# Kernel optimization log

Measured on AMD Instinct MI355X. Metric: run time of the kernel, lower is better.

Reference implementation:

```python
import jax, jax.numpy as jnp
import numpy as np

NEG_SLOPE = 0.2  # PyG GATConv default negative_slope

def gat_layer(x, src, dst, W, a_src, a_dst, bias, n_nodes):
    # x: [N, F_in]; W: [F_in, H*C]; a_src/a_dst: [H, C]; bias: [H*C]
    H, C = a_src.shape
    h = (x @ W).reshape(n_nodes, H, C)                      # [N, H, C]
    al_src = jnp.sum(h * a_src, axis=-1)                    # [N, H]
    al_dst = jnp.sum(h * a_dst, axis=-1)                    # [N, H]
    e = jax.nn.leaky_relu(al_src[src] + al_dst[dst], NEG_SLOPE)  # [E, H]
    # segment softmax over destination nodes (every node has a self loop)
    m = jax.ops.segment_max(e, dst, num_segments=n_nodes)  # [N, H]
    ex = jnp.exp(e - m[dst])
    denom = jax.ops.segment_sum(ex, dst, num_segments=n_nodes)  # [N, H]
    alpha = ex / denom[dst]                                 # [E, H]
    out = jax.ops.segment_sum(h[src] * alpha[:, :, None], dst, num_segments=n_nodes)  # [N, H, C]
    return out.reshape(n_nodes, H * C) + bias


def setup_inputs() -> dict:
    key = jax.random.key(0)
    ks = jax.random.split(key, 10)
    N, E, F_in, H, Ch, Co = 50000, 800000, 128, 4, 32, 8
    s = lambda fan: 1.0 / np.sqrt(fan)
    return {
        "x": jax.random.normal(ks[0], (N, F_in), dtype=jnp.float32),
        "edge_index": jax.random.randint(ks[1], (2, E), 0, N, dtype=jnp.int64),
        "W1": jax.random.normal(ks[2], (F_in, H * Ch), dtype=jnp.float32) * s(F_in),
        "att_src1": jax.random.normal(ks[3], (H, Ch), dtype=jnp.float32) * s(Ch),
        "att_dst1": jax.random.normal(ks[4], (H, Ch), dtype=jnp.float32) * s(Ch),
        "bias1": jnp.zeros((H * Ch,), dtype=jnp.float32),
        "W2": jax.random.normal(ks[5], (H * Ch, H * Co), dtype=jnp.float32) * s(H * Ch),
        "att_src2": jax.random.normal(ks[6], (H, Co), dtype=jnp.float32) * s(Co),
        "att_dst2": jax.random.normal(ks[7], (H, Co), dtype=jnp.float32) * s(Co),
        "bias2": jnp.zeros((H * Co,), dtype=jnp.float32),
    }


def reference(x, edge_index, W1, att_src1, att_dst1, bias1, W2, att_src2, att_dst2, bias2):
    n = x.shape[0]
    loop = jnp.arange(n, dtype=edge_index.dtype)  # add_self_loops=True (PyG default)
    src = jnp.concatenate([edge_index[0], loop])
    dst = jnp.concatenate([edge_index[1], loop])
    h = jax.nn.relu(gat_layer(x, src, dst, W1, att_src1, att_dst1, bias1, n))
    # F.dropout(p=0.6, training=False) -> identity in eval mode
    out = gat_layer(h, src, dst, W2, att_src2, att_dst2, bias2, n)
    return jax.nn.log_softmax(out, axis=1)
```

## Files before the change

### kernel.cpp

```cpp
#include <hip/hip_runtime.h>
#include <hip/hip_fp16.h>

struct alignas(8) Half4 { __half2 lo; __half2 hi; };

#define MAXDEG 64


__global__ void k_fill(const int* __restrict__ ei, int E, int N,
                       int* __restrict__ cursor, unsigned short* __restrict__ adj) {
  int e = blockIdx.x * blockDim.x + threadIdx.x;
  int Et = E + N;
  if (e >= Et) return;
  int s, d;
  if (e < E) { s = ei[e]; d = ei[E + e]; } else { s = d = e - E; }
  int pos = atomicAdd(&cursor[d], 1);
  if (pos < MAXDEG) adj[(size_t)d * MAXDEG + pos] = (unsigned short)s;
}


#define XS_STRIDE 33

__global__ void __launch_bounds__(256) k_gemm1(
    const float* __restrict__ x, const float* __restrict__ W,
    const float* __restrict__ as, const float* __restrict__ ad,
    __half* __restrict__ h1h, float* __restrict__ als,
    float* __restrict__ ald, int N) {
  __shared__ float4 xs[64 * XS_STRIDE];
  int t = threadIdx.x;
  int base = blockIdx.x * 64;
  const float4* x4 = (const float4*)x;
  #pragma unroll
  for (int i = 0; i < 8; ++i) {
    int idx = t + i * 256;
    int n = idx >> 5, k4 = idx & 31;
    int gn = base + n; if (gn >= N) gn = N - 1;
    xs[n * XS_STRIDE + k4] = x4[gn * 32 + k4];
  }
  __syncthreads();

  int c4 = t & 31, nr = t >> 5;
  const float4* w4 = (const float4*)W;
  float4 acc[8];
  #pragma unroll
  for (int i = 0; i < 8; ++i) acc[i] = make_float4(0.f, 0.f, 0.f, 0.f);

  for (int k4 = 0; k4 < 32; ++k4) {
    float4 w0 = w4[(k4 * 4 + 0) * 32 + c4];
    float4 w1 = w4[(k4 * 4 + 1) * 32 + c4];
    float4 w2 = w4[(k4 * 4 + 2) * 32 + c4];
    float4 w3 = w4[(k4 * 4 + 3) * 32 + c4];
    #pragma unroll
    for (int i = 0; i < 8; ++i) {
      float4 xv = xs[(nr * 8 + i) * XS_STRIDE + k4];
      acc[i].x += xv.x * w0.x + xv.y * w1.x + xv.z * w2.x + xv.w * w3.x;
      acc[i].y += xv.x * w0.y + xv.y * w1.y + xv.z * w2.y + xv.w * w3.y;
      acc[i].z += xv.x * w0.z + xv.y * w1.z + xv.z * w2.z + xv.w * w3.z;
      acc[i].w += xv.x * w0.w + xv.y * w1.w + xv.z * w2.w + xv.w * w3.w;
    }
  }

  int hh = c4 >> 3;
  int cl = (c4 & 7) * 4;
  float a10 = as[hh * 32 + cl], a11 = as[hh * 32 + cl + 1],
        a12 = as[hh * 32 + cl + 2], a13 = as[hh * 32 + cl + 3];
  float a20 = ad[hh * 32 + cl], a21 = ad[hh * 32 + cl + 1],
        a22 = ad[hh * 32 + cl + 2], a23 = ad[hh * 32 + cl + 3];
  Half4* h1p = (Half4*)h1h;
  #pragma unroll
  for (int i = 0; i < 8; ++i) {
    int gn = base + nr * 8 + i;
    float ps = acc[i].x * a10 + acc[i].y * a11 + acc[i].z * a12 + acc[i].w * a13;
    float pd = acc[i].x * a20 + acc[i].y * a21 + acc[i].z * a22 + acc[i].w * a23;
    ps += __shfl_xor(ps, 1); pd += __shfl_xor(pd, 1);
    ps += __shfl_xor(ps, 2); pd += __shfl_xor(pd, 2);
    ps += __shfl_xor(ps, 4); pd += __shfl_xor(pd, 4);
    if (gn < N) {
      Half4 hv;
      hv.lo = __floats2half2_rn(acc[i].x, acc[i].y);
      hv.hi = __floats2half2_rn(acc[i].z, acc[i].w);
      h1p[gn * 32 + c4] = hv;
      if ((c4 & 7) == 0) { als[gn * 4 + hh] = ps; ald[gn * 4 + hh] = pd; }
    }
  }
}


__global__ void __launch_bounds__(256) k_gemm2(
    const __half* __restrict__ hin, const float* __restrict__ W,
    const float* __restrict__ as, const float* __restrict__ ad,
    __half* __restrict__ h2h, float* __restrict__ als,
    float* __restrict__ ald, int N) {
  __shared__ float4 xs[64 * XS_STRIDE];
  __shared__ float2 ws[128 * 16];
  int t = threadIdx.x;
  int base = blockIdx.x * 64;
  const uint2* xg = (const uint2*)hin;
  #pragma unroll
  for (int i = 0; i < 8; ++i) {
    int idx = t + i * 256;
    int n = idx >> 5, k4 = idx & 31;
    int gn = base + n; if (gn >= N) gn = N - 1;
    uint2 u = xg[gn * 32 + k4];
    __half2 a = *(const __half2*)&u.x;
    __half2 b = *(const __half2*)&u.y;
    float2 fa = __half22float2(a), fb = __half22float2(b);
    xs[n * XS_STRIDE + k4] = make_float4(fa.x, fa.y, fb.x, fb.y);
  }
  const float2* w2g = (const float2*)W;
  #pragma unroll
  for (int i = 0; i < 8; ++i) ws[t + i * 256] = w2g[t + i * 256];
  __syncthreads();

  int c2 = t & 15, nr = t >> 4;
  float2 acc[4];
  #pragma unroll
  for (int i = 0; i < 4; ++i) acc[i] = make_float2(0.f, 0.f);

  #pragma unroll 4
  for (int k4 = 0; k4 < 32; ++k4) {
    float2 w0 = ws[(k4 * 4 + 0) * 16 + c2];
    float2 w1 = ws[(k4 * 4 + 1) * 16 + c2];
    float2 w2v = ws[(k4 * 4 + 2) * 16 + c2];
    float2 w3 = ws[(k4 * 4 + 3) * 16 + c2];
    #pragma unroll
    for (int i = 0; i < 4; ++i) {
      float4 xv = xs[(nr * 4 + i) * XS_STRIDE + k4];
      acc[i].x += xv.x * w0.x + xv.y * w1.x + xv.z * w2v.x + xv.w * w3.x;
      acc[i].y += xv.x * w0.y + xv.y * w1.y + xv.z * w2v.y + xv.w * w3.y;
    }
  }

  int hh = c2 >> 2;
  int cl = (c2 & 3) * 2;
  float a10 = as[hh * 8 + cl], a11 = as[hh * 8 + cl + 1];
  float a20 = ad[hh * 8 + cl], a21 = ad[hh * 8 + cl + 1];
  __half2* h2p = (__half2*)h2h;
  #pragma unroll
  for (int i = 0; i < 4; ++i) {
    int gn = base + nr * 4 + i;
    float ps = acc[i].x * a10 + acc[i].y * a11;
    float pd = acc[i].x * a20 + acc[i].y * a21;
    ps += __shfl_xor(ps, 1); pd += __shfl_xor(pd, 1);
    ps += __shfl_xor(ps, 2); pd += __shfl_xor(pd, 2);
    if (gn < N) {
      h2p[gn * 16 + c2] = __floats2half2_rn(acc[i].x, acc[i].y);
      if ((c2 & 3) == 0) { als[gn * 4 + hh] = ps; ald[gn * 4 + hh] = pd; }
    }
  }
}


__global__ void k_agg1(const int* __restrict__ degp, const unsigned short* __restrict__ adj,
                       const __half* __restrict__ h1h, const float* __restrict__ als,
                       const float* __restrict__ ald, const float* __restrict__ bias,
                       __half* __restrict__ outh, int N) {
  int wid = (blockIdx.x * blockDim.x + threadIdx.x) >> 6;
  int lane = threadIdx.x & 63;
  if (wid >= N) return;
  int h = lane >> 4;
  int hb = h * 4;
  int jw = lane & 3, hw = (lane >> 2) & 3;
  float aldw = ald[wid * 4 + hw];
  float aldo = ald[wid * 4 + h];
  int deg = degp[wid]; if (deg > MAXDEG) deg = MAXDEG;
  const unsigned short* arow = adj + (size_t)wid * MAXDEG;
  float acc0 = 0.f, acc1 = 0.f, wsum = 0.f;
  const __half2* h1v = (const __half2*)h1h;
  int p = 0;
  for (; p + 3 < deg; p += 4) {
    int sj = arow[p + jw];
    int s0 = __shfl(sj, 0), s1 = __shfl(sj, 1), s2 = __shfl(sj, 2), s3 = __shfl(sj, 3);
    float2 v0 = __half22float2(h1v[s0 * 64 + lane]);
    float2 v1 = __half22float2(h1v[s1 * 64 + lane]);
    float2 v2 = __half22float2(h1v[s2 * 64 + lane]);
    float2 v3 = __half22float2(h1v[s3 * 64 + lane]);
    float ew = als[sj * 4 + hw] + aldw;
    ew = (ew > 0.f) ? ew : 0.2f * ew;
    float w = __expf(ew);
    float w0 = __shfl(w, hb + 0), w1 = __shfl(w, hb + 1),
          w2 = __shfl(w, hb + 2), w3 = __shfl(w, hb + 3);
    wsum += (w0 + w1) + (w2 + w3);
    acc0 += w0 * v0.x + w1 * v1.x + w2 * v2.x + w3 * v3.x;
    acc1 += w0 * v0.y + w1 * v1.y + w2 * v2.y + w3 * v3.y;
  }
  for (; p < deg; ++p) {
    int s0 = arow[p];
    float e0 = als[s0 * 4 + h] + aldo;
    e0 = (e0 > 0.f) ? e0 : 0.2f * e0;
    float w0 = __expf(e0);
    float2 v0 = __half22float2(h1v[s0 * 64 + lane]);
    wsum += w0;
    acc0 += w0 * v0.x;
    acc1 += w0 * v0.y;
  }
  float inv = 1.f / wsum;
  float o0 = fmaxf(acc0 * inv + bias[lane * 2 + 0], 0.f);
  float o1 = fmaxf(acc1 * inv + bias[lane * 2 + 1], 0.f);
  ((__half2*)outh)[wid * 64 + lane] = __floats2half2_rn(o0, o1);
}


__global__ void k_agg2(const int* __restrict__ degp, const unsigned short* __restrict__ adj,
                       const __half* __restrict__ h2h, const float* __restrict__ als,
                       const float* __restrict__ ald, const float* __restrict__ bias,
                       float* __restrict__ out, int N) {
  int tid = blockIdx.x * blockDim.x + threadIdx.x;
  int node = tid >> 5;
  int sl = threadIdx.x & 31;
  if (node >= N) return;
  int h = sl >> 3;
  int hb = h * 4;
  int jw = sl & 3, hw = (sl >> 2) & 3;
  float aldw = ald[node * 4 + hw];
  float aldo = ald[node * 4 + h];
  int deg = degp[node]; if (deg > MAXDEG) deg = MAXDEG;
  const unsigned short* arow = adj + (size_t)node * MAXDEG;
  float acc = 0.f, wsum = 0.f;
  int p = 0;
  for (; p + 3 < deg; p += 4) {
    int sj = arow[p + jw];
    int s0 = __shfl(sj, 0, 32), s1 = __shfl(sj, 1, 32),
        s2 = __shfl(sj, 2, 32), s3 = __shfl(sj, 3, 32);
    float x0 = __half2float(h2h[s0 * 32 + sl]);
    float x1 = __half2float(h2h[s1 * 32 + sl]);
    float x2 = __half2float(h2h[s2 * 32 + sl]);
    float x3 = __half2float(h2h[s3 * 32 + sl]);
    float ew = als[sj * 4 + hw] + aldw;
    ew = (ew > 0.f) ? ew : 0.2f * ew;
    float w = __expf(ew);
    float w0 = __shfl(w, hb + 0, 32), w1 = __shfl(w, hb + 1, 32),
          w2 = __shfl(w, hb + 2, 32), w3 = __shfl(w, hb + 3, 32);
    wsum += (w0 + w1) + (w2 + w3);
    acc += (w0 * x0 + w1 * x1) + (w2 * x2 + w3 * x3);
  }
  for (; p < deg; ++p) {
    int s0 = arow[p];
    float e0 = als[s0 * 4 + h] + aldo;
    e0 = (e0 > 0.f) ? e0 : 0.2f * e0;
    float w0 = __expf(e0);
    wsum += w0;
    acc += w0 * __half2float(h2h[s0 * 32 + sl]);
  }
  float val = acc / wsum + bias[sl];
  float m = val;
  for (int off = 16; off; off >>= 1) m = fmaxf(m, __shfl_xor(m, off, 32));
  float ex = __expf(val - m);
  float ssum = ex;
  for (int off = 16; off; off >>= 1) ssum += __shfl_xor(ssum, off, 32);
  out[node * 32 + sl] = val - m - __logf(ssum);
}


extern "C" void kernel_launch(void* const* d_in, const int* in_sizes, int n_in,
                              void* d_out, int out_size, void* d_ws, size_t ws_size,
                              hipStream_t stream) {
  const float* x   = (const float*)d_in[0];
  const int*   ei  = (const int*)d_in[1];
  const float* W1  = (const float*)d_in[2];
  const float* as1 = (const float*)d_in[3];
  const float* ad1 = (const float*)d_in[4];
  const float* b1  = (const float*)d_in[5];
  const float* W2  = (const float*)d_in[6];
  const float* as2 = (const float*)d_in[7];
  const float* ad2 = (const float*)d_in[8];
  const float* b2  = (const float*)d_in[9];
  float* outp = (float*)d_out;

  int N  = in_sizes[0] / 128;
  int E  = in_sizes[1] / 2;
  int Et = E + N;

  char* wsp = (char*)d_ws;
  size_t off = 0;
  auto alloc = [&](size_t bytes) -> void* {
    void* p = wsp + off;
    off += (bytes + 255) & ~(size_t)255;
    return p;
  };
  int*            cursor = (int*)alloc((size_t)N * 4);
  unsigned short* adj    = (unsigned short*)alloc((size_t)N * MAXDEG * 2);
  __half*         h1     = (__half*)alloc((size_t)N * 128 * 2);
  float*          al1s   = (float*)alloc((size_t)N * 4 * 4);
  float*          al1d   = (float*)alloc((size_t)N * 4 * 4);
  __half*         h2in   = (__half*)alloc((size_t)N * 128 * 2);
  __half*         h2     = (__half*)alloc((size_t)N * 32 * 2);
  float*          al2s   = (float*)alloc((size_t)N * 4 * 4);
  float*          al2d   = (float*)alloc((size_t)N * 4 * 4);

  hipMemsetAsync(cursor, 0, (size_t)N * 4, stream);

  int eb = (Et + 255) / 256;
  k_fill<<<eb, 256, 0, stream>>>(ei, E, N, cursor, adj);

  int gb = (N + 63) / 64;
  k_gemm1<<<gb, 256, 0, stream>>>(x, W1, as1, ad1, h1, al1s, al1d, N);
  k_agg1 <<<(N + 3) / 4, 256, 0, stream>>>(cursor, adj, h1, al1s, al1d, b1, h2in, N);
  k_gemm2<<<gb, 256, 0, stream>>>(h2in, W2, as2, ad2, h2, al2s, al2d, N);
  k_agg2 <<<(N + 7) / 8, 256, 0, stream>>>(cursor, adj, h2, al2s, al2d, b2, outp, N);
}
```

Measured before the change: 177.5 us.

## Fuse adjacency fill into gemm1 and layer-1 aggregation into gemm2

Adjacency construction runs as extra blocks of the first GEMM launch, removing a separate launch. Layer-1 aggregation is computed per block into shared memory and fed directly into the layer-2 GEMM, removing the h2in intermediate round trip through global memory and one launch. In exchange, each wave now aggregates 16 nodes serially, which reduces the number of independent gather waves in flight.

```diff
diff --git a/kernel.cpp b/kernel.cpp
--- a/kernel.cpp
+++ b/kernel.cpp
@@ -4,30 +4,32 @@
 struct alignas(8) Half4 { __half2 lo; __half2 hi; };
 
 #define MAXDEG 64
-
-
-__global__ void k_fill(const int* __restrict__ ei, int E, int N,
-                       int* __restrict__ cursor, unsigned short* __restrict__ adj) {
-  int e = blockIdx.x * blockDim.x + threadIdx.x;
-  int Et = E + N;
-  if (e >= Et) return;
-  int s, d;
-  if (e < E) { s = ei[e]; d = ei[E + e]; } else { s = d = e - E; }
-  int pos = atomicAdd(&cursor[d], 1);
-  if (pos < MAXDEG) adj[(size_t)d * MAXDEG + pos] = (unsigned short)s;
-}
-
-
 #define XS_STRIDE 33
 
-__global__ void __launch_bounds__(256) k_gemm1(
+
+__global__ void __launch_bounds__(256) k_fg1(
+    const int* __restrict__ ei, int E, int N, int gb,
+    int* __restrict__ cursor, unsigned short* __restrict__ adj,
     const float* __restrict__ x, const float* __restrict__ W,
     const float* __restrict__ as, const float* __restrict__ ad,
-    __half* __restrict__ h1h, float* __restrict__ als,
-    float* __restrict__ ald, int N) {
+    __half* __restrict__ h1h, float* __restrict__ als, float* __restrict__ ald) {
   __shared__ float4 xs[64 * XS_STRIDE];
+  int b = blockIdx.x;
   int t = threadIdx.x;
-  int base = blockIdx.x * 64;
+
+  if (b >= gb) {
+    int e = (b - gb) * 256 + t;
+    int Et = E + N;
+    if (e < Et) {
+      int s, d;
+      if (e < E) { s = ei[e]; d = ei[E + e]; } else { s = d = e - E; }
+      int pos = atomicAdd(&cursor[d], 1);
+      if (pos < MAXDEG) adj[(size_t)d * MAXDEG + pos] = (unsigned short)s;
+    }
+    return;
+  }
+
+  int base = b * 64;
   const float4* x4 = (const float4*)x;
   #pragma unroll
   for (int i = 0; i < 8; ++i) {
@@ -85,30 +87,71 @@
 }
 
 
-__global__ void __launch_bounds__(256) k_gemm2(
-    const __half* __restrict__ hin, const float* __restrict__ W,
-    const float* __restrict__ as, const float* __restrict__ ad,
-    __half* __restrict__ h2h, float* __restrict__ als,
-    float* __restrict__ ald, int N) {
+__global__ void __launch_bounds__(256) k_ag12(
+    const int* __restrict__ degp, const unsigned short* __restrict__ adj,
+    const __half* __restrict__ h1h, const float* __restrict__ als1,
+    const float* __restrict__ ald1, const float* __restrict__ b1,
+    const float* __restrict__ W2,
+    const float* __restrict__ as2, const float* __restrict__ ad2,
+    __half* __restrict__ h2h, float* __restrict__ als2,
+    float* __restrict__ ald2, int N) {
   __shared__ float4 xs[64 * XS_STRIDE];
   __shared__ float2 ws[128 * 16];
   int t = threadIdx.x;
   int base = blockIdx.x * 64;
-  const uint2* xg = (const uint2*)hin;
-  #pragma unroll
-  for (int i = 0; i < 8; ++i) {
-    int idx = t + i * 256;
-    int n = idx >> 5, k4 = idx & 31;
-    int gn = base + n; if (gn >= N) gn = N - 1;
-    uint2 u = xg[gn * 32 + k4];
-    __half2 a = *(const __half2*)&u.x;
-    __half2 b = *(const __half2*)&u.y;
-    float2 fa = __half22float2(a), fb = __half22float2(b);
-    xs[n * XS_STRIDE + k4] = make_float4(fa.x, fa.y, fb.x, fb.y);
-  }
-  const float2* w2g = (const float2*)W;
+
+  const float2* w2g = (const float2*)W2;
   #pragma unroll
   for (int i = 0; i < 8; ++i) ws[t + i * 256] = w2g[t + i * 256];
+
+  int lane = t & 63, wv = t >> 6;
+  int h = lane >> 4;
+  int hb = h * 4;
+  int jw = lane & 3, hw = (lane >> 2) & 3;
+  const __half2* h1v = (const __half2*)h1h;
+  float2* xs2 = (float2*)xs;
+  float bs0 = b1[lane * 2 + 0], bs1 = b1[lane * 2 + 1];
+
+  for (int i = 0; i < 16; ++i) {
+    int ln = wv * 16 + i;
+    int node = base + ln; if (node >= N) node = N - 1;
+    float aldw = ald1[node * 4 + hw];
+    float aldo = ald1[node * 4 + h];
+    int deg = degp[node]; if (deg > MAXDEG) deg = MAXDEG;
+    const unsigned short* arow = adj + (size_t)node * MAXDEG;
+    float acc0 = 0.f, acc1 = 0.f, wsum = 0.f;
+    int p = 0;
+    for (; p + 3 < deg; p += 4) {
+      int sj = arow[p + jw];
+      int s0 = __shfl(sj, 0), s1 = __shfl(sj, 1), s2 = __shfl(sj, 2), s3 = __shfl(sj, 3);
+      float2 v0 = __half22float2(h1v[s0 * 64 + lane]);
+      float2 v1 = __half22float2(h1v[s1 * 64 + lane]);
+      float2 v2 = __half22float2(h1v[s2 * 64 + lane]);
+      float2 v3 = __half22float2(h1v[s3 * 64 + lane]);
+      float ew = als1[sj * 4 + hw] + aldw;
+      ew = (ew > 0.f) ? ew : 0.2f * ew;
+      float w = __expf(ew);
+      float w0 = __shfl(w, hb + 0), w1 = __shfl(w, hb + 1),
+            w2 = __shfl(w, hb + 2), w3 = __shfl(w, hb + 3);
+      wsum += (w0 + w1) + (w2 + w3);
+      acc0 += w0 * v0.x + w1 * v1.x + w2 * v2.x + w3 * v3.x;
+      acc1 += w0 * v0.y + w1 * v1.y + w2 * v2.y + w3 * v3.y;
+    }
+    for (; p < deg; ++p) {
+      int s0 = arow[p];
+      float e0 = als1[s0 * 4 + h] + aldo;
+      e0 = (e0 > 0.f) ? e0 : 0.2f * e0;
+      float w0 = __expf(e0);
+      float2 v0 = __half22float2(h1v[s0 * 64 + lane]);
+      wsum += w0;
+      acc0 += w0 * v0.x;
+      acc1 += w0 * v0.y;
+    }
+    float inv = 1.f / wsum;
+    float o0 = fmaxf(acc0 * inv + bs0, 0.f);
+    float o1 = fmaxf(acc1 * inv + bs1, 0.f);
+    xs2[ln * 66 + lane] = make_float2(o0, o1);
+  }
   __syncthreads();
 
   int c2 = t & 15, nr = t >> 4;
@@ -132,8 +175,8 @@
 
   int hh = c2 >> 2;
   int cl = (c2 & 3) * 2;
-  float a10 = as[hh * 8 + cl], a11 = as[hh * 8 + cl + 1];
-  float a20 = ad[hh * 8 + cl], a21 = ad[hh * 8 + cl + 1];
+  float a10 = as2[hh * 8 + cl], a11 = as2[hh * 8 + cl + 1];
+  float a20 = ad2[hh * 8 + cl], a21 = ad2[hh * 8 + cl + 1];
   __half2* h2p = (__half2*)h2h;
   #pragma unroll
   for (int i = 0; i < 4; ++i) {
@@ -144,59 +187,9 @@
     ps += __shfl_xor(ps, 2); pd += __shfl_xor(pd, 2);
     if (gn < N) {
       h2p[gn * 16 + c2] = __floats2half2_rn(acc[i].x, acc[i].y);
-      if ((c2 & 3) == 0) { als[gn * 4 + hh] = ps; ald[gn * 4 + hh] = pd; }
-    }
-  }
-}
-
-
-__global__ void k_agg1(const int* __restrict__ degp, const unsigned short* __restrict__ adj,
-                       const __half* __restrict__ h1h, const float* __restrict__ als,
-                       const float* __restrict__ ald, const float* __restrict__ bias,
-                       __half* __restrict__ outh, int N) {
-  int wid = (blockIdx.x * blockDim.x + threadIdx.x) >> 6;
-  int lane = threadIdx.x & 63;
-  if (wid >= N) return;
-  int h = lane >> 4;
-  int hb = h * 4;
-  int jw = lane & 3, hw = (lane >> 2) & 3;
-  float aldw = ald[wid * 4 + hw];
-  float aldo = ald[wid * 4 + h];
-  int deg = degp[wid]; if (deg > MAXDEG) deg = MAXDEG;
-  const unsigned short* arow = adj + (size_t)wid * MAXDEG;
-  float acc0 = 0.f, acc1 = 0.f, wsum = 0.f;
-  const __half2* h1v = (const __half2*)h1h;
-  int p = 0;
-  for (; p + 3 < deg; p += 4) {
-    int sj = arow[p + jw];
-    int s0 = __shfl(sj, 0), s1 = __shfl(sj, 1), s2 = __shfl(sj, 2), s3 = __shfl(sj, 3);
-    float2 v0 = __half22float2(h1v[s0 * 64 + lane]);
-    float2 v1 = __half22float2(h1v[s1 * 64 + lane]);
-    float2 v2 = __half22float2(h1v[s2 * 64 + lane]);
-    float2 v3 = __half22float2(h1v[s3 * 64 + lane]);
-    float ew = als[sj * 4 + hw] + aldw;
-    ew = (ew > 0.f) ? ew : 0.2f * ew;
-    float w = __expf(ew);
-    float w0 = __shfl(w, hb + 0), w1 = __shfl(w, hb + 1),
-          w2 = __shfl(w, hb + 2), w3 = __shfl(w, hb + 3);
-    wsum += (w0 + w1) + (w2 + w3);
-    acc0 += w0 * v0.x + w1 * v1.x + w2 * v2.x + w3 * v3.x;
-    acc1 += w0 * v0.y + w1 * v1.y + w2 * v2.y + w3 * v3.y;
-  }
-  for (; p < deg; ++p) {
-    int s0 = arow[p];
-    float e0 = als[s0 * 4 + h] + aldo;
-    e0 = (e0 > 0.f) ? e0 : 0.2f * e0;
-    float w0 = __expf(e0);
-    float2 v0 = __half22float2(h1v[s0 * 64 + lane]);
-    wsum += w0;
-    acc0 += w0 * v0.x;
-    acc1 += w0 * v0.y;
-  }
-  float inv = 1.f / wsum;
-  float o0 = fmaxf(acc0 * inv + bias[lane * 2 + 0], 0.f);
-  float o1 = fmaxf(acc1 * inv + bias[lane * 2 + 1], 0.f);
-  ((__half2*)outh)[wid * 64 + lane] = __floats2half2_rn(o0, o1);
+      if ((c2 & 3) == 0) { als2[gn * 4 + hh] = ps; ald2[gn * 4 + hh] = pd; }
+    }
+  }
 }
 
 
@@ -282,19 +275,17 @@
   __half*         h1     = (__half*)alloc((size_t)N * 128 * 2);
   float*          al1s   = (float*)alloc((size_t)N * 4 * 4);
   float*          al1d   = (float*)alloc((size_t)N * 4 * 4);
-  __half*         h2in   = (__half*)alloc((size_t)N * 128 * 2);
   __half*         h2     = (__half*)alloc((size_t)N * 32 * 2);
   float*          al2s   = (float*)alloc((size_t)N * 4 * 4);
   float*          al2d   = (float*)alloc((size_t)N * 4 * 4);
 
   hipMemsetAsync(cursor, 0, (size_t)N * 4, stream);
 
+  int gb = (N + 63) / 64;
   int eb = (Et + 255) / 256;
-  k_fill<<<eb, 256, 0, stream>>>(ei, E, N, cursor, adj);
-
-  int gb = (N + 63) / 64;
-  k_gemm1<<<gb, 256, 0, stream>>>(x, W1, as1, ad1, h1, al1s, al1d, N);
-  k_agg1 <<<(N + 3) / 4, 256, 0, stream>>>(cursor, adj, h1, al1s, al1d, b1, h2in, N);
-  k_gemm2<<<gb, 256, 0, stream>>>(h2in, W2, as2, ad2, h2, al2s, al2d, N);
-  k_agg2 <<<(N + 7) / 8, 256, 0, stream>>>(cursor, adj, h2, al2s, al2d, b2, outp, N);
-}
+  k_fg1<<<gb + eb, 256, 0, stream>>>(ei, E, N, gb, cursor, adj,
+                                     x, W1, as1, ad1, h1, al1s, al1d);
+  k_ag12<<<gb, 256, 0, stream>>>(cursor, adj, h1, al1s, al1d, b1,
+                                 W2, as2, ad2, h2, al2s, al2d, N);
+  k_agg2<<<(N + 7) / 8, 256, 0, stream>>>(cursor, adj, h2, al2s, al2d, b2, outp, N);
+}
```

Result: slower. 230.0 us (+29.6%).
